# Kernel optimization log

Measured on AMD Instinct MI355X. Metric: run time of the kernel, lower is better.

## Reference

```python
import jax, jax.numpy as jnp
import numpy as np

N = 100000   # nodes
E = 1600000  # edges
IN, H, C = 128, 128, 40


def setup_inputs() -> dict:
    key = jax.random.key(0)
    ks = jax.random.split(key, 8)
    feat = jax.random.normal(ks[0], (N, IN), jnp.float32)
    src = jax.random.randint(ks[1], (E,), 0, N, jnp.int32)
    dst = jax.random.randint(ks[2], (E,), 0, N, jnp.int32)
    # Glorot-ish init like dgl GraphConv.reset_parameters
    W0 = jax.random.normal(ks[3], (IN, H), jnp.float32) * (1.0 / np.sqrt(IN))
    W1 = jax.random.normal(ks[4], (H, H), jnp.float32) * (1.0 / np.sqrt(H))
    W2 = jax.random.normal(ks[5], (H, C), jnp.float32) * (1.0 / np.sqrt(H))
    b0 = jnp.zeros((H,), jnp.float32)
    b1 = jnp.zeros((H,), jnp.float32)
    b2 = jnp.zeros((C,), jnp.float32)
    return {"feat": feat, "src": src, "dst": dst,
            "W0": W0, "b0": b0, "W1": W1, "b1": b1, "W2": W2, "b2": b2}


def _graph_conv(h, src, dst, W, b):
    # dgl GraphConv with norm='both': D_out^{-1/2} pre-scale, sum-aggregate,
    # D_in^{-1/2} post-scale; degrees clamped to min 1. Weight applied before
    # aggregation (in_feats >= out_feats path) -- math is identical either way.
    ones = jnp.ones((src.shape[0],), h.dtype)
    deg_out = jnp.maximum(jax.ops.segment_sum(ones, src, num_segments=N), 1.0)
    deg_in = jnp.maximum(jax.ops.segment_sum(ones, dst, num_segments=N), 1.0)
    h = h * (deg_out ** -0.5)[:, None]
    h = h @ W                                   # [N, out]
    agg = jax.ops.segment_sum(h[src], dst, num_segments=N)  # gather+scatter
    return agg * (deg_in ** -0.5)[:, None] + b


def reference(feat, src, dst, W0, b0, W1, b1, W2, b2):
    h = jax.nn.relu(_graph_conv(feat, src, dst, W0, b0))  # dropout p=0 -> identity
    h = jax.nn.relu(_graph_conv(h, src, dst, W1, b1))
    return _graph_conv(h, src, dst, W2, b2)
```

## Files before the change

kernel.cpp:

```cpp
#include <hip/hip_runtime.h>

#define NN 100000
#define EE 1600000
#define ELLW 64
#define GEMMN ((NN + 31) / 32)
#define BQ ((EE / 4 + 511) / 512)
#define GRID_BG (BQ * 5)

typedef int iv4 __attribute__((ext_vector_type(4)));

__device__ __forceinline__ unsigned int pack_bf2(float a, float b) {
    unsigned int ua = __float_as_uint(a);
    ua += 0x7FFFu + ((ua >> 16) & 1u);
    unsigned int ub = __float_as_uint(b);
    ub += 0x7FFFu + ((ub >> 16) & 1u);
    return (ua >> 16) | (ub & 0xFFFF0000u);
}

__device__ __forceinline__ void gemm128_body(const float* __restrict__ X,
                                             const float* __restrict__ W, unsigned int* __restrict__ Y,
                                             int row0, int tid, float* Xs) {
    const float4* X4 = (const float4*)X;
#pragma unroll
    for (int idx = tid; idx < 1024; idx += 256) {
        int r = idx & 31, c4 = idx >> 5;
        int row = row0 + r;
        float4 v = X4[(size_t)row * 32 + c4];
        Xs[(c4 * 4 + 0) * 32 + r] = v.x;
        Xs[(c4 * 4 + 1) * 32 + r] = v.y;
        Xs[(c4 * 4 + 2) * 32 + r] = v.z;
        Xs[(c4 * 4 + 3) * 32 + r] = v.w;
    }
    __syncthreads();
    int cg = tid & 31;
    int rg = tid >> 5;
    float a[4][4];
#pragma unroll
    for (int r = 0; r < 4; ++r)
#pragma unroll
        for (int c = 0; c < 4; ++c) a[r][c] = 0.f;
    const float4* W4 = (const float4*)W;
#pragma unroll 4
    for (int k = 0; k < 128; ++k) {
        float4 xv = *(const float4*)&Xs[k * 32 + rg * 4];
        float4 wv = W4[k * 32 + cg];
        float xr[4] = {xv.x, xv.y, xv.z, xv.w};
        float wc[4] = {wv.x, wv.y, wv.z, wv.w};
#pragma unroll
        for (int r = 0; r < 4; ++r)
#pragma unroll
            for (int c = 0; c < 4; ++c) a[r][c] = fmaf(xr[r], wc[c], a[r][c]);
    }
    int rbase = row0 + rg * 4;
    uint2* Y2 = (uint2*)Y;
#pragma unroll
    for (int r = 0; r < 4; ++r) {
        Y2[(size_t)(rbase + r) * 32 + cg] =
            make_uint2(pack_bf2(a[r][0], a[r][1]), pack_bf2(a[r][2], a[r][3]));
    }
}

__global__ __launch_bounds__(256) void k_build_gemm0(const int* __restrict__ src, const int* __restrict__ dst,
                                                     int* __restrict__ din, int* __restrict__ dout,
                                                     int* __restrict__ ell,
                                                     const float* __restrict__ X, const float* __restrict__ W,
                                                     unsigned int* __restrict__ Y) {
    __shared__ float Xs[128 * 32];
    int tid = threadIdx.x;
    int q = blockIdx.x / 5, rem = blockIdx.x % 5;
    if (rem) {
        int g = q * 4 + (rem - 1);
        if (g < GEMMN) gemm128_body(X, W, Y, g * 32, tid, Xs);
        return;
    }
    const iv4* s4p = (const iv4*)src;
    const iv4* d4p = (const iv4*)dst;
    const int n4 = EE / 4;
#pragma unroll
    for (int h = 0; h < 2; ++h) {
        int i4 = q * 512 + h * 256 + tid;
        if (i4 < n4) {
            iv4 s4 = __builtin_nontemporal_load(&s4p[i4]);
            iv4 d4 = __builtin_nontemporal_load(&d4p[i4]);
            int ss[4] = {s4.x, s4.y, s4.z, s4.w};
            int dd[4] = {d4.x, d4.y, d4.z, d4.w};
#pragma unroll
            for (int k = 0; k < 4; ++k) {
                int p = atomicAdd(&din[dd[k]], 1);
                if (p < ELLW) ell[(size_t)dd[k] * ELLW + p] = ss[k];
            }
#pragma unroll
            for (int k = 0; k < 4; ++k) atomicAdd(&dout[ss[k]], 1);
        }
    }
}

__global__ __launch_bounds__(256) void k_gathergemm128(const unsigned int* __restrict__ h,
                                                       const int* __restrict__ din, const int* __restrict__ dout,
                                                       const int* __restrict__ ell,
                                                       const float* __restrict__ bias,
                                                       const float* __restrict__ W,
                                                       unsigned int* __restrict__ Y, int so_mode) {
    __shared__ float Xs[128 * 36];
    int tid = threadIdx.x;
    int wv = tid >> 6, lane = tid & 63;
    int row0 = blockIdx.x * 32;
    float2 bb = ((const float2*)bias)[lane];
    for (int j8 = 0; j8 < 8; ++j8) {
        int r = wv * 8 + j8;
        int v = row0 + r;
        int dv = din[v];
        int cnt = min(dv, ELLW);
        int cl = ell[(size_t)v * ELLW + lane];
        int cls = (lane < cnt) ? cl : 0;
        float scl = 1.f;
        if (so_mode) scl = rsqrtf((float)max(1, dout[cls]));
        float sx = 0.f, sy = 0.f;
        for (int j = 0; j < cnt; j += 8) {
            int cc[8]; float mk[8]; unsigned int t[8];
#pragma unroll
            for (int k = 0; k < 8; ++k) {
                int jj = j + k;
                int jc = jj < cnt ? jj : cnt - 1;
                cc[k] = __shfl(cls, jc);
                float sw = so_mode ? __shfl(scl, jc) : 1.f;
                mk[k] = (jj < cnt) ? sw : 0.f;
            }
#pragma unroll
            for (int k = 0; k < 8; ++k) t[k] = h[(size_t)cc[k] * 64 + lane];
#pragma unroll
            for (int k = 0; k < 8; ++k) {
                float x = __uint_as_float(t[k] << 16);
                float y = __uint_as_float(t[k] & 0xFFFF0000u);
                sx = fmaf(mk[k], x, sx);
                sy = fmaf(mk[k], y, sy);
            }
        }
        float si = rsqrtf((float)max(1, dv));
        float so = rsqrtf((float)max(1, dout[v]));
        float ox = fmaxf(sx * si + bb.x, 0.f) * so;
        float oy = fmaxf(sy * si + bb.y, 0.f) * so;
        Xs[(2 * lane) * 36 + r] = ox;
        Xs[(2 * lane + 1) * 36 + r] = oy;
    }
    __syncthreads();
    int cg = tid & 31, rg = tid >> 5;
    float a[4][4];
#pragma unroll
    for (int r = 0; r < 4; ++r)
#pragma unroll
        for (int c = 0; c < 4; ++c) a[r][c] = 0.f;
    const float4* W4 = (const float4*)W;
#pragma unroll 4
    for (int k = 0; k < 128; ++k) {
        float4 xv = *(const float4*)&Xs[k * 36 + rg * 4];
        float4 wv4 = W4[k * 32 + cg];
        float xr[4] = {xv.x, xv.y, xv.z, xv.w};
        float wc[4] = {wv4.x, wv4.y, wv4.z, wv4.w};
#pragma unroll
        for (int r = 0; r < 4; ++r)
#pragma unroll
            for (int c = 0; c < 4; ++c) a[r][c] = fmaf(xr[r], wc[c], a[r][c]);
    }
    int rbase = row0 + rg * 4;
    uint2* Y2 = (uint2*)Y;
#pragma unroll
    for (int r = 0; r < 4; ++r) {
        Y2[(size_t)(rbase + r) * 32 + cg] =
            make_uint2(pack_bf2(a[r][0], a[r][1]), pack_bf2(a[r][2], a[r][3]));
    }
}

__global__ __launch_bounds__(256) void k_gathergemm40(const unsigned int* __restrict__ h,
                                                      const int* __restrict__ din, const int* __restrict__ dout,
                                                      const int* __restrict__ ell,
                                                      const float* __restrict__ bias,
                                                      const float* __restrict__ W,
                                                      unsigned int* __restrict__ Y) {
    __shared__ float Xs[128 * 36];
    __shared__ float Os[32 * 40];
    int tid = threadIdx.x;
    int wv = tid >> 6, lane = tid & 63;
    int row0 = blockIdx.x * 32;
    float2 bb = ((const float2*)bias)[lane];
    for (int j8 = 0; j8 < 8; ++j8) {
        int r = wv * 8 + j8;
        int v = row0 + r;
        int dv = din[v];
        int cnt = min(dv, ELLW);
        int cl = ell[(size_t)v * ELLW + lane];
        int cls = (lane < cnt) ? cl : 0;
        float sx = 0.f, sy = 0.f;
        for (int j = 0; j < cnt; j += 8) {
            int cc[8]; float mk[8]; unsigned int t[8];
#pragma unroll
            for (int k = 0; k < 8; ++k) {
                int jj = j + k;
                cc[k] = __shfl(cls, jj < cnt ? jj : cnt - 1);
                mk[k] = (jj < cnt) ? 1.f : 0.f;
            }
#pragma unroll
            for (int k = 0; k < 8; ++k) t[k] = h[(size_t)cc[k] * 64 + lane];
#pragma unroll
            for (int k = 0; k < 8; ++k) {
                float x = __uint_as_float(t[k] << 16);
                float y = __uint_as_float(t[k] & 0xFFFF0000u);
                sx = fmaf(mk[k], x, sx);
                sy = fmaf(mk[k], y, sy);
            }
        }
        float si = rsqrtf((float)max(1, dv));
        float so = rsqrtf((float)max(1, dout[v]));
        float ox = fmaxf(sx * si + bb.x, 0.f) * so;
        float oy = fmaxf(sy * si + bb.y, 0.f) * so;
        Xs[(2 * lane) * 36 + r] = ox;
        Xs[(2 * lane + 1) * 36 + r] = oy;
    }
    __syncthreads();
    int rg = tid >> 3;
    int cg = tid & 7;
    float a[5] = {0.f, 0.f, 0.f, 0.f, 0.f};
    for (int k = 0; k < 128; ++k) {
        float x = Xs[k * 36 + rg];
#pragma unroll
        for (int c = 0; c < 5; ++c) a[c] = fmaf(x, W[k * 40 + cg * 5 + c], a[c]);
    }
#pragma unroll
    for (int c = 0; c < 5; ++c) Os[rg * 40 + cg * 5 + c] = a[c];
    __syncthreads();
    for (int i = tid; i < 640; i += 256) {
        int row = i / 20, pj = i % 20;
        Y[(size_t)(row0 + row) * 32 + pj] = pack_bf2(Os[row * 40 + 2 * pj], Os[row * 40 + 2 * pj + 1]);
    }
}

__global__ __launch_bounds__(256) void k_gather40(const unsigned short* __restrict__ h, const int* __restrict__ din,
                                                  const int* __restrict__ ell,
                                                  const float* __restrict__ b, float* __restrict__ out, int n) {
    int wv = threadIdx.x >> 6, lane = threadIdx.x & 63;
    int v = blockIdx.x * 4 + wv;
    if (v >= n) return;
    int dv = din[v];
    int cnt = min(dv, ELLW);
    int cl = ell[(size_t)v * ELLW + lane];
    int cls = (lane < cnt) ? cl : 0;
    float s = 0.f;
    for (int j = 0; j < cnt; j += 8) {
        int cc[8]; float mk[8]; unsigned short t[8];
#pragma unroll
        for (int k = 0; k < 8; ++k) {
            int jj = j + k;
            cc[k] = __shfl(cls, jj < cnt ? jj : cnt - 1);
            mk[k] = (jj < cnt) ? 1.f : 0.f;
        }
        if (lane < 40) {
#pragma unroll
            for (int k = 0; k < 8; ++k) t[k] = h[(size_t)cc[k] * 64 + lane];
#pragma unroll
            for (int k = 0; k < 8; ++k)
                s = fmaf(mk[k], __uint_as_float((unsigned int)t[k] << 16), s);
        }
    }
    if (lane < 40) {
        out[(size_t)v * 40 + lane] = s * rsqrtf((float)max(1, dv)) + b[lane];
    }
}

extern "C" void kernel_launch(void* const* d_in, const int* in_sizes, int n_in,
                              void* d_out, int out_size, void* d_ws, size_t ws_size,
                              hipStream_t stream) {
    const float* feat = (const float*)d_in[0];
    const int*   src  = (const int*)d_in[1];
    const int*   dst  = (const int*)d_in[2];
    const float* W0   = (const float*)d_in[3];
    const float* b0   = (const float*)d_in[4];
    const float* W1   = (const float*)d_in[5];
    const float* b1   = (const float*)d_in[6];
    const float* W2   = (const float*)d_in[7];
    const float* b2   = (const float*)d_in[8];
    float* out = (float*)d_out;

    char* w = (char*)d_ws;
    int*   din       = (int*)w;    w += (size_t)NN * 4;
    int*   dout      = (int*)w;    w += (size_t)NN * 4;
    int*   ell       = (int*)w;    w += (size_t)NN * ELLW * 4;
    unsigned int* h2 = (unsigned int*)w; w += (size_t)NN * 128 * 2;
    unsigned int* h2b = (unsigned int*)w; w += (size_t)NN * 128 * 2;
    unsigned int* h40 = (unsigned int*)w; w += (size_t)NN * 32 * 4;

    (void)hipMemsetAsync(d_ws, 0, (size_t)NN * 8, stream);

    k_build_gemm0<<<GRID_BG, 256, 0, stream>>>(src, dst, din, dout, ell, feat, W0, h2);
    k_gathergemm128<<<GEMMN, 256, 0, stream>>>(h2, din, dout, ell, b0, W1, h2b, 1);
    k_gathergemm40<<<GEMMN, 256, 0, stream>>>(h2b, din, dout, ell, b1, W2, h40);
    k_gather40<<<(NN + 3) / 4, 256, 0, stream>>>((const unsigned short*)h40, din, ell, b2, out, NN);
}
```

Measured before the change: 553.2 us.

## Build ELL via two-pass bucketed staging with shared-memory atomics

Replaces scattered global atomics on per-node degree counters with a two-pass scheme. The first pass bins edges into 512-node buckets using shared-memory histograms and per-bucket global offsets, writing packed staging arrays. A second kernel then builds per-node counts and the ELL table with shared-memory atomics, one bucket per block. This is meant to cut the cost of contended random global atomics, at the price of an extra launch, extra staging traffic, and fixed bucket capacities that could overflow on skewed graphs.

```diff
diff --git a/kernel.cpp b/kernel.cpp
--- a/kernel.cpp
+++ b/kernel.cpp
@@ -6,6 +6,11 @@
 #define GEMMN ((NN + 31) / 32)
 #define BQ ((EE / 4 + 511) / 512)
 #define GRID_BG (BQ * 5)
+
+#define NBKT 196
+#define BSH 9
+#define CAPD 10240
+#define CAPS 10240
 
 typedef int iv4 __attribute__((ext_vector_type(4)));
 
@@ -60,11 +65,12 @@
     }
 }
 
-__global__ __launch_bounds__(256) void k_build_gemm0(const int* __restrict__ src, const int* __restrict__ dst,
-                                                     int* __restrict__ din, int* __restrict__ dout,
-                                                     int* __restrict__ ell,
-                                                     const float* __restrict__ X, const float* __restrict__ W,
-                                                     unsigned int* __restrict__ Y) {
+__global__ __launch_bounds__(256) void k_buildA_gemm0(const int* __restrict__ src, const int* __restrict__ dst,
+                                                      int* __restrict__ curD, int* __restrict__ curS,
+                                                      unsigned int* __restrict__ stagD,
+                                                      unsigned short* __restrict__ stagS,
+                                                      const float* __restrict__ X, const float* __restrict__ W,
+                                                      unsigned int* __restrict__ Y) {
     __shared__ float Xs[128 * 32];
     int tid = threadIdx.x;
     int q = blockIdx.x / 5, rem = blockIdx.x % 5;
@@ -73,24 +79,101 @@
         if (g < GEMMN) gemm128_body(X, W, Y, g * 32, tid, Xs);
         return;
     }
+    int* sh = (int*)Xs;
+    for (int i = tid; i < 1536; i += 256) sh[i] = 0;
+    __syncthreads();
+
     const iv4* s4p = (const iv4*)src;
     const iv4* d4p = (const iv4*)dst;
     const int n4 = EE / 4;
+    iv4 sv[2], dv[2];
+    int have[2];
 #pragma unroll
     for (int h = 0; h < 2; ++h) {
         int i4 = q * 512 + h * 256 + tid;
-        if (i4 < n4) {
-            iv4 s4 = __builtin_nontemporal_load(&s4p[i4]);
-            iv4 d4 = __builtin_nontemporal_load(&d4p[i4]);
-            int ss[4] = {s4.x, s4.y, s4.z, s4.w};
-            int dd[4] = {d4.x, d4.y, d4.z, d4.w};
+        have[h] = (i4 < n4);
+        if (have[h]) {
+            sv[h] = __builtin_nontemporal_load(&s4p[i4]);
+            dv[h] = __builtin_nontemporal_load(&d4p[i4]);
+        }
+    }
+#pragma unroll
+    for (int h = 0; h < 2; ++h) {
+        if (have[h]) {
+            int ss[4] = {sv[h].x, sv[h].y, sv[h].z, sv[h].w};
+            int dd[4] = {dv[h].x, dv[h].y, dv[h].z, dv[h].w};
 #pragma unroll
             for (int k = 0; k < 4; ++k) {
-                int p = atomicAdd(&din[dd[k]], 1);
-                if (p < ELLW) ell[(size_t)dd[k] * ELLW + p] = ss[k];
-            }
-#pragma unroll
-            for (int k = 0; k < 4; ++k) atomicAdd(&dout[ss[k]], 1);
+                atomicAdd(&sh[dd[k] >> BSH], 1);
+                atomicAdd(&sh[256 + (ss[k] >> BSH)], 1);
+            }
+        }
+    }
+    __syncthreads();
+    if (tid < NBKT) {
+        int hd = sh[tid];
+        sh[512 + tid] = hd ? atomicAdd(&curD[tid], hd) : 0;
+        int hs = sh[256 + tid];
+        sh[768 + tid] = hs ? atomicAdd(&curS[tid], hs) : 0;
+    }
+    __syncthreads();
+#pragma unroll
+    for (int h = 0; h < 2; ++h) {
+        if (have[h]) {
+            int ss[4] = {sv[h].x, sv[h].y, sv[h].z, sv[h].w};
+            int dd[4] = {dv[h].x, dv[h].y, dv[h].z, dv[h].w};
+#pragma unroll
+            for (int k = 0; k < 4; ++k) {
+                int bd = dd[k] >> BSH;
+                int od = atomicAdd(&sh[1024 + bd], 1);
+                stagD[(size_t)bd * CAPD + sh[512 + bd] + od] =
+                    ((unsigned int)ss[k] << BSH) | (unsigned int)(dd[k] & 511);
+                int bs = ss[k] >> BSH;
+                int os = atomicAdd(&sh[1280 + bs], 1);
+                stagS[(size_t)bs * CAPS + sh[768 + bs] + os] = (unsigned short)(ss[k] & 511);
+            }
+        }
+    }
+}
+
+__global__ __launch_bounds__(256) void k_buildB(const int* __restrict__ curD, const int* __restrict__ curS,
+                                                const unsigned int* __restrict__ stagD,
+                                                const unsigned short* __restrict__ stagS,
+                                                int* __restrict__ din, int* __restrict__ dout,
+                                                int* __restrict__ ell) {
+    __shared__ int cl[512];
+    int tid = threadIdx.x;
+    int b = blockIdx.x;
+    for (int i = tid; i < 512; i += 256) cl[i] = 0;
+    __syncthreads();
+    if (b < NBKT) {
+        int n0 = b << BSH;
+        int cnt = min(curD[b], CAPD);
+        const unsigned int* sg = stagD + (size_t)b * CAPD;
+        for (int i = tid; i < cnt; i += 256) {
+            unsigned int v = sg[i];
+            int dlow = (int)(v & 511u);
+            int s = (int)(v >> BSH);
+            int p = atomicAdd(&cl[dlow], 1);
+            if (p < ELLW) ell[(size_t)(n0 + dlow) * ELLW + p] = s;
+        }
+        __syncthreads();
+        for (int i = tid; i < 512; i += 256) {
+            int node = n0 + i;
+            if (node < NN) din[node] = cl[i];
+        }
+    } else {
+        int bs = b - NBKT;
+        int n0 = bs << BSH;
+        int cnt = min(curS[bs], CAPS);
+        const unsigned short* sg = stagS + (size_t)bs * CAPS;
+        for (int i = tid; i < cnt; i += 256) {
+            atomicAdd(&cl[sg[i]], 1);
+        }
+        __syncthreads();
+        for (int i = tid; i < 512; i += 256) {
+            int node = n0 + i;
+            if (node < NN) dout[node] = cl[i];
         }
     }
 }
@@ -283,14 +366,19 @@
     char* w = (char*)d_ws;
     int*   din       = (int*)w;    w += (size_t)NN * 4;
     int*   dout      = (int*)w;    w += (size_t)NN * 4;
+    int*   curD      = (int*)w;    w += 256 * 4;
+    int*   curS      = (int*)w;    w += 256 * 4;
     int*   ell       = (int*)w;    w += (size_t)NN * ELLW * 4;
+    unsigned int*   stagD = (unsigned int*)w;   w += (size_t)NBKT * CAPD * 4;
+    unsigned short* stagS = (unsigned short*)w; w += (size_t)NBKT * CAPS * 2;
     unsigned int* h2 = (unsigned int*)w; w += (size_t)NN * 128 * 2;
     unsigned int* h2b = (unsigned int*)w; w += (size_t)NN * 128 * 2;
     unsigned int* h40 = (unsigned int*)w; w += (size_t)NN * 32 * 4;
 
-    (void)hipMemsetAsync(d_ws, 0, (size_t)NN * 8, stream);
-
-    k_build_gemm0<<<GRID_BG, 256, 0, stream>>>(src, dst, din, dout, ell, feat, W0, h2);
+    (void)hipMemsetAsync(d_ws, 0, (size_t)NN * 8 + 2048, stream);
+
+    k_buildA_gemm0<<<GRID_BG, 256, 0, stream>>>(src, dst, curD, curS, stagD, stagS, feat, W0, h2);
+    k_buildB<<<NBKT * 2, 256, 0, stream>>>(curD, curS, stagD, stagS, din, dout, ell);
     k_gathergemm128<<<GEMMN, 256, 0, stream>>>(h2, din, dout, ell, b0, W1, h2b, 1);
     k_gathergemm40<<<GEMMN, 256, 0, stream>>>(h2b, din, dout, ell, b1, W2, h40);
     k_gather40<<<(NN + 3) / 4, 256, 0, stream>>>((const unsigned short*)h40, din, ell, b2, out, NN);
```

Measured after the change: 491.9 us. 1.12x faster.
